# Performance work log

Measured on AMD Instinct MI355X. Metric: run time of the kernel, lower is better.

Reference implementation:

```python
import jax, jax.numpy as jnp
import numpy as np

N = 100000
E = 1600000
D_IN = 128
F = 128


def _glorot(key, shape, scale=1.0):
    fan_in, fan_out = shape
    std = jnp.sqrt(2.0 / (fan_in + fan_out))
    return jax.random.normal(key, shape, dtype=jnp.float32) * std * scale


def setup_inputs() -> dict:
    key = jax.random.key(0)
    ks = jax.random.split(key, 10)
    h = jax.random.normal(ks[0], (N, D_IN), dtype=jnp.float32)
    # ensure every node appears as a row (src) so degree >= 1 (no inf in deg**-0.5)
    src_extra = jax.random.randint(ks[1], (E - N,), 0, N, dtype=jnp.int32)
    edge_src = jnp.concatenate([jnp.arange(N, dtype=jnp.int32), src_extra])
    edge_dst = jax.random.randint(ks[2], (E,), 0, N, dtype=jnp.int32)
    # faithful to original: fake indices sampled in [0, E) (jnp indexing clamps)
    src_fake = jax.random.randint(ks[3], (E,), 0, E, dtype=jnp.int32)
    dst_fake = jax.random.randint(ks[4], (E,), 0, E, dtype=jnp.int32)
    w_gcn0 = _glorot(ks[5], (D_IN, F))
    w_gcn1 = _glorot(ks[6], (F, F))
    # small scale on rate0 head to keep exp(sum over F dims) finite in fp32
    w_rate0 = _glorot(ks[7], (F, F), scale=0.05)
    w_rate1 = _glorot(ks[8], (F, 1))
    w_alpha = _glorot(ks[9], (F, 1))
    return {"h": h, "w_gcn0": w_gcn0, "w_gcn1": w_gcn1, "w_rate0": w_rate0,
            "w_rate1": w_rate1, "w_alpha": w_alpha, "edge_src": edge_src,
            "edge_dst": edge_dst, "src_fake": src_fake, "dst_fake": dst_fake}


def _gcn(h, W, norm, edge_src, edge_dst):
    h = h * norm                     # [N, d] degree pre-norm
    h = h @ W                        # dense projection
    h = jax.ops.segment_sum(h[edge_dst], edge_src, num_segments=N)  # a @ h
    return h * norm                  # degree post-norm


def reference(h, w_gcn0, w_gcn1, w_rate0, w_rate1, w_alpha,
              edge_src, edge_dst, src_fake, dst_fake):
    ones = jnp.ones((E,), dtype=h.dtype)
    deg = jax.ops.segment_sum(ones, edge_src, num_segments=N)  # row sums of a
    norm = (deg ** -0.5)[:, None]

    h = _gcn(h, w_gcn0, norm, edge_src, edge_dst)
    h = _gcn(h, w_gcn1, norm, edge_src, edge_dst)

    rate0 = h @ w_rate0   # [N, F]
    rate1 = h @ w_rate1   # [N, 1]
    alpha = h @ w_alpha   # [N, 1]

    src, dst = edge_src, edge_dst
    rate0_real = jnp.exp((rate0[src] + rate0[dst]).sum(-1))
    rate1_real = jnp.exp((rate1[src] + rate1[dst]).sum(-1))
    alpha_real = jax.nn.sigmoid((alpha[src] * alpha[dst]).sum(-1) / alpha.shape[-1] ** 0.5)

    # faithful to original (including rate0+rate1 mix and /shape (not sqrt) in alpha_fake)
    rate0_fake = jnp.exp((rate0[src_fake] + rate1[dst_fake]).sum(-1))
    rate1_fake = jnp.exp((rate1[src_fake] + rate1[dst_fake]).sum(-1))
    alpha_fake = jax.nn.sigmoid((alpha[src] * alpha[dst_fake]).sum(-1) / alpha.shape[-1])

    return jnp.stack([rate0_real, rate1_real, alpha_real,
                      rate0_fake, rate1_fake, alpha_fake])  # [6, E]
```

## Files before the change

### kernel.cpp

```cpp
#include <hip/hip_runtime.h>
#include <math.h>

#define NN 100000
#define EE 1600000
#define KB 256
#define RR 391
#define CAP 8192


__global__ __launch_bounds__(1024) void k_pmat(const float* __restrict__ w_gcn0,
                                               const float* __restrict__ w_gcn1,
                                               const float* __restrict__ w_rate0,
                                               const float* __restrict__ w_rate1,
                                               const float* __restrict__ w_alpha,
                                               float* __restrict__ Pt0, float* __restrict__ Pt1,
                                               float* __restrict__ Pt2, int* __restrict__ gcur) {
    __shared__ float V0[128], V1[128], V2[128];
    __shared__ float Q0[128], Q1[128], Q2[128];
    int t = threadIdx.x;
    if (t < KB) gcur[t] = 0;
    int r = t >> 3, seg = t & 7;
    {
        const float* p = w_rate0 + r * 128 + seg * 16;
        float s = 0.f;
        #pragma unroll
        for (int k = 0; k < 16; ++k) s += p[k];
        s += __shfl_down(s, 4, 8); s += __shfl_down(s, 2, 8); s += __shfl_down(s, 1, 8);
        if (seg == 0) V0[r] = s;
    }
    if (t < 128) { V1[t] = w_rate1[t]; V2[t] = w_alpha[t]; }
    __syncthreads();
    {
        const float* p = w_gcn1 + r * 128 + seg * 16;
        float q0 = 0.f, q1 = 0.f, q2 = 0.f;
        #pragma unroll
        for (int k = 0; k < 16; ++k) {
            float w = p[k]; int j = seg * 16 + k;
            q0 += w * V0[j]; q1 += w * V1[j]; q2 += w * V2[j];
        }
        q0 += __shfl_down(q0, 4, 8); q0 += __shfl_down(q0, 2, 8); q0 += __shfl_down(q0, 1, 8);
        q1 += __shfl_down(q1, 4, 8); q1 += __shfl_down(q1, 2, 8); q1 += __shfl_down(q1, 1, 8);
        q2 += __shfl_down(q2, 4, 8); q2 += __shfl_down(q2, 2, 8); q2 += __shfl_down(q2, 1, 8);
        if (seg == 0) { Q0[r] = q0; Q1[r] = q1; Q2[r] = q2; }
    }
    __syncthreads();
    {
        const float* p = w_gcn0 + r * 128 + seg * 16;
        float q0 = 0.f, q1 = 0.f, q2 = 0.f;
        #pragma unroll
        for (int k = 0; k < 16; ++k) {
            float w = p[k]; int j = seg * 16 + k;
            q0 += w * Q0[j]; q1 += w * Q1[j]; q2 += w * Q2[j];
        }
        q0 += __shfl_down(q0, 4, 8); q0 += __shfl_down(q0, 2, 8); q0 += __shfl_down(q0, 1, 8);
        q1 += __shfl_down(q1, 4, 8); q1 += __shfl_down(q1, 2, 8); q1 += __shfl_down(q1, 1, 8);
        q2 += __shfl_down(q2, 4, 8); q2 += __shfl_down(q2, 2, 8); q2 += __shfl_down(q2, 1, 8);
        if (seg == 0) { Pt0[r] = q0; Pt1[r] = q1; Pt2[r] = q2; }
    }
}


__global__ __launch_bounds__(256) void k_part(const int* __restrict__ src, const int* __restrict__ dst,
                                              int* __restrict__ gcur, unsigned int* __restrict__ pk, int E) {
    __shared__ int cnt[KB];
    __shared__ int base[KB];
    int t = threadIdx.x;
    int e0 = blockIdx.x * 2048;
    cnt[t] = 0;
    __syncthreads();
    unsigned int pkv[8];
    int bkt[8];
    #pragma unroll
    for (int i = 0; i < 8; ++i) {
        int e = e0 + i * 256 + t;
        if (e < E) {
            int s = src[e];
            int d = dst[e];
            int b = s / RR;
            bkt[i] = b;
            pkv[i] = (unsigned int)d | ((unsigned int)(s - b * RR) << 17);
            atomicAdd(&cnt[b], 1);
        } else bkt[i] = -1;
    }
    __syncthreads();
    base[t] = cnt[t] ? atomicAdd(&gcur[t], cnt[t]) : 0;
    __syncthreads();
    cnt[t] = 0;
    __syncthreads();
    #pragma unroll
    for (int i = 0; i < 8; ++i) {
        if (bkt[i] >= 0) {
            int rr = atomicAdd(&cnt[bkt[i]], 1);
            int rel = base[bkt[i]] + rr;
            if (rel < CAP) pk[bkt[i] * CAP + rel] = pkv[i];
        }
    }
}


__global__ __launch_bounds__(1024) void k_cnt_proj(const unsigned int* __restrict__ pk,
                                                   const int* __restrict__ gcur,
                                                   const float* __restrict__ h,
                                                   const float* __restrict__ Pt0, const float* __restrict__ Pt1,
                                                   const float* __restrict__ Pt2,
                                                   float* __restrict__ nrm, float4* __restrict__ w4) {
    __shared__ int c[RR];
    __shared__ float s_nrm[RR];
    __shared__ float sP0[128], sP1[128], sP2[128];
    int b = blockIdx.x;
    int t = threadIdx.x;
    int nlo = b * RR;
    int nn = NN - nlo; if (nn > RR) nn = RR;
    if (nn <= 0) return;
    if (t < 128) { sP0[t] = Pt0[t]; sP1[t] = Pt1[t]; sP2[t] = Pt2[t]; }
    if (t < RR) c[t] = 0;
    __syncthreads();
    int P0 = b * CAP;
    int m = gcur[b]; if (m > CAP) m = CAP;
    for (int i = t; i < m; i += 1024) atomicAdd(&c[pk[P0 + i] >> 17], 1);
    __syncthreads();
    if (t < nn) {
        float nv = rsqrtf((float)c[t]);
        s_nrm[t] = nv;
        nrm[nlo + t] = nv;
    }
    __syncthreads();
    int hw = t >> 5;
    int l32 = t & 31;
    int c4 = l32 * 4;
    float4 c0 = *(const float4*)(sP0 + c4);
    float4 c1 = *(const float4*)(sP1 + c4);
    float4 c2 = *(const float4*)(sP2 + c4);
    for (int i0 = 0; i0 < nn; i0 += 32) {
        int i = i0 + hw;
        if (i >= nn) break;
        int node = nlo + i;
        float4 hv = *(const float4*)(h + (size_t)node * 128 + c4);
        float p0v = hv.x * c0.x + hv.y * c0.y + hv.z * c0.z + hv.w * c0.w;
        float p1v = hv.x * c1.x + hv.y * c1.y + hv.z * c1.z + hv.w * c1.w;
        float p2v = hv.x * c2.x + hv.y * c2.y + hv.z * c2.z + hv.w * c2.w;
        #pragma unroll
        for (int off = 16; off > 0; off >>= 1) {
            p0v += __shfl_down(p0v, off, 32);
            p1v += __shfl_down(p1v, off, 32);
            p2v += __shfl_down(p2v, off, 32);
        }
        if (l32 == 0) {
            float nv = s_nrm[i];
            w4[node] = make_float4(nv * p0v, nv * p1v, nv * p2v, 0.f);
        }
    }
}


template<int MODE>
__global__ __launch_bounds__(1024) void k_agg(const unsigned int* __restrict__ pk,
                                              const int* __restrict__ gcur,
                                              const float4* __restrict__ T, const float* __restrict__ nrm,
                                              float4* __restrict__ outv) {
    __shared__ float s0[RR], s1[RR], s2[RR];
    int b = blockIdx.x;
    int t = threadIdx.x;
    int nlo = b * RR;
    int nn = NN - nlo; if (nn > RR) nn = RR;
    if (nn <= 0) return;
    if (t < RR) { s0[t] = 0.f; s1[t] = 0.f; s2[t] = 0.f; }
    __syncthreads();
    int P0 = b * CAP;
    int m = gcur[b]; if (m > CAP) m = CAP;
    for (int i = t; i < m; i += 1024) {
        unsigned int w = pk[P0 + i];
        float4 v = T[w & 0x1FFFFu];
        int srel = (int)(w >> 17);
        atomicAdd(&s0[srel], v.x);
        atomicAdd(&s1[srel], v.y);
        atomicAdd(&s2[srel], v.z);
    }
    __syncthreads();
    for (int i = t; i < nn; i += 1024) {
        int node = nlo + i;
        float nv = nrm[node];
        float sc = (MODE == 1) ? nv * nv : nv;
        outv[node] = make_float4(sc * s0[i], sc * s1[i], sc * s2[i], 0.f);
    }
}


__global__ __launch_bounds__(256) void k_edge(const int* __restrict__ esrc, const int* __restrict__ edst,
                                              const int* __restrict__ sfake, const int* __restrict__ dfake,
                                              const float4* __restrict__ p4, float* __restrict__ out, int E) {
    int t = threadIdx.x;
    int e00 = blockIdx.x * 512 + t;
    #pragma unroll
    for (int k = 0; k < 2; ++k) {
        int e = e00 + k * 256;
        if (e < E) {
            int s = esrc[e], d = edst[e];
            int sf = sfake[e]; sf = sf < 0 ? 0 : (sf >= NN ? NN - 1 : sf);
            int df = dfake[e]; df = df < 0 ? 0 : (df >= NN ? NN - 1 : df);
            float4 ps = p4[s], pd = p4[d], psf = p4[sf], pdf = p4[df];
            out[e]                  = expf(ps.x + pd.x);
            out[(size_t)EE + e]     = expf(ps.y + pd.y);
            out[(size_t)2 * EE + e] = 1.f / (1.f + expf(-(ps.z * pd.z)));
            out[(size_t)3 * EE + e] = expf(psf.x + 128.f * pdf.y);
            out[(size_t)4 * EE + e] = expf(psf.y + pdf.y);
            out[(size_t)5 * EE + e] = 1.f / (1.f + expf(-(ps.z * pdf.z)));
        }
    }
}


extern "C" void kernel_launch(void* const* d_in, const int* in_sizes, int n_in,
                              void* d_out, int out_size, void* d_ws, size_t ws_size,
                              hipStream_t stream) {
    const float* h       = (const float*)d_in[0];
    const float* w_gcn0  = (const float*)d_in[1];
    const float* w_gcn1  = (const float*)d_in[2];
    const float* w_rate0 = (const float*)d_in[3];
    const float* w_rate1 = (const float*)d_in[4];
    const float* w_alpha = (const float*)d_in[5];
    const int* edge_src  = (const int*)d_in[6];
    const int* edge_dst  = (const int*)d_in[7];
    const int* src_fake  = (const int*)d_in[8];
    const int* dst_fake  = (const int*)d_in[9];
    float* out = (float*)d_out;

    const int E = EE;

    char* p = (char*)d_ws;
    auto alloc = [&](size_t bytes) {
        char* r = p;
        p += (bytes + 255) & ~(size_t)255;
        return r;
    };
    unsigned int* pk = (unsigned int*)alloc((size_t)KB * CAP * 4);
    int* gcur   = (int*)alloc(KB * 4);
    float* nrm  = (float*)alloc((size_t)NN * 4);
    float4* w4  = (float4*)alloc((size_t)NN * 16);
    float4* z4  = (float4*)alloc((size_t)NN * 16);
    float4* p4  = (float4*)alloc((size_t)NN * 16);
    float* Pt0  = (float*)alloc(512);
    float* Pt1  = (float*)alloc(512);
    float* Pt2  = (float*)alloc(512);

    k_pmat<<<1, 1024, 0, stream>>>(w_gcn0, w_gcn1, w_rate0, w_rate1, w_alpha, Pt0, Pt1, Pt2, gcur);
    k_part<<<(E + 2047) / 2048, 256, 0, stream>>>(edge_src, edge_dst, gcur, pk, E);
    k_cnt_proj<<<KB, 1024, 0, stream>>>(pk, gcur, h, Pt0, Pt1, Pt2, nrm, w4);
    k_agg<1><<<KB, 1024, 0, stream>>>(pk, gcur, w4, nrm, z4);
    k_agg<2><<<KB, 1024, 0, stream>>>(pk, gcur, z4, nrm, p4);
    k_edge<<<(E + 511) / 512, 256, 0, stream>>>(edge_src, edge_dst, src_fake, dst_fake, p4, out, E);
}
```

Baseline: 235.8 us.

## Overlap edge partition with h projection; vectorize edge kernel I/O

The edge partitioning and the h-projection now run in one launch, with blocks alternating between the two roles so the 51 MB h read overlaps the edge bucketing. Since the norm is not known yet at that point, it is stored in the w lane of u4 by the count kernel and applied inside the first aggregation. The aggregation loop is unrolled by two to keep more gathers in flight. The edge kernel uses int4 index loads and float4 output stores. The merged kernel removes the serial h read from the count kernel, but adds a branch per block and an extra multiply per gathered edge.

```diff
diff --git a/kernel.cpp b/kernel.cpp
--- a/kernel.cpp
+++ b/kernel.cpp
@@ -60,95 +60,103 @@
 }
 
 
-__global__ __launch_bounds__(256) void k_part(const int* __restrict__ src, const int* __restrict__ dst,
-                                              int* __restrict__ gcur, unsigned int* __restrict__ pk, int E) {
-    __shared__ int cnt[KB];
-    __shared__ int base[KB];
-    int t = threadIdx.x;
-    int e0 = blockIdx.x * 2048;
-    cnt[t] = 0;
-    __syncthreads();
-    unsigned int pkv[8];
-    int bkt[8];
-    #pragma unroll
-    for (int i = 0; i < 8; ++i) {
-        int e = e0 + i * 256 + t;
-        if (e < E) {
-            int s = src[e];
-            int d = dst[e];
-            int b = s / RR;
-            bkt[i] = b;
-            pkv[i] = (unsigned int)d | ((unsigned int)(s - b * RR) << 17);
-            atomicAdd(&cnt[b], 1);
-        } else bkt[i] = -1;
-    }
-    __syncthreads();
-    base[t] = cnt[t] ? atomicAdd(&gcur[t], cnt[t]) : 0;
-    __syncthreads();
-    cnt[t] = 0;
-    __syncthreads();
-    #pragma unroll
-    for (int i = 0; i < 8; ++i) {
-        if (bkt[i] >= 0) {
-            int rr = atomicAdd(&cnt[bkt[i]], 1);
-            int rel = base[bkt[i]] + rr;
-            if (rel < CAP) pk[bkt[i] * CAP + rel] = pkv[i];
-        }
-    }
-}
-
-
-__global__ __launch_bounds__(1024) void k_cnt_proj(const unsigned int* __restrict__ pk,
-                                                   const int* __restrict__ gcur,
+__global__ __launch_bounds__(512) void k_part_proj(const int* __restrict__ src, const int* __restrict__ dst,
+                                                   int* __restrict__ gcur, unsigned int* __restrict__ pk,
                                                    const float* __restrict__ h,
                                                    const float* __restrict__ Pt0, const float* __restrict__ Pt1,
                                                    const float* __restrict__ Pt2,
-                                                   float* __restrict__ nrm, float4* __restrict__ w4) {
+                                                   float4* __restrict__ u4) {
+    __shared__ int cnt[KB];
+    __shared__ int base[KB];
+    __shared__ float sP0[128], sP1[128], sP2[128];
+    int t = threadIdx.x;
+    int role = blockIdx.x & 1;
+    int id = blockIdx.x >> 1;
+
+    if (role == 0) {
+        if (t < KB) cnt[t] = 0;
+        __syncthreads();
+        int e0 = id * 4096;
+        unsigned int pkv[8];
+        int bkt[8];
+        #pragma unroll
+        for (int i = 0; i < 8; ++i) {
+            int e = e0 + i * 512 + t;
+            if (e < EE) {
+                int s = src[e];
+                int d = dst[e];
+                int b = s / RR;
+                bkt[i] = b;
+                pkv[i] = (unsigned int)d | ((unsigned int)(s - b * RR) << 17);
+                atomicAdd(&cnt[b], 1);
+            } else bkt[i] = -1;
+        }
+        __syncthreads();
+        if (t < KB) base[t] = cnt[t] ? atomicAdd(&gcur[t], cnt[t]) : 0;
+        __syncthreads();
+        if (t < KB) cnt[t] = 0;
+        __syncthreads();
+        #pragma unroll
+        for (int i = 0; i < 8; ++i) {
+            if (bkt[i] >= 0) {
+                int rr = atomicAdd(&cnt[bkt[i]], 1);
+                int rel = base[bkt[i]] + rr;
+                if (rel < CAP) pk[bkt[i] * CAP + rel] = pkv[i];
+            }
+        }
+    } else {
+        if (t < 128) { sP0[t] = Pt0[t]; sP1[t] = Pt1[t]; sP2[t] = Pt2[t]; }
+        __syncthreads();
+        int hw = t >> 5;
+        int l32 = t & 31;
+        int c4 = l32 * 4;
+        float4 c0 = *(const float4*)(sP0 + c4);
+        float4 c1 = *(const float4*)(sP1 + c4);
+        float4 c2 = *(const float4*)(sP2 + c4);
+        int nlo = id * 256;
+        for (int i0 = 0; i0 < 256; i0 += 16) {
+            int node = nlo + i0 + hw;
+            if (node < NN) {
+                float4 hv = *(const float4*)(h + (size_t)node * 128 + c4);
+                float p0v = hv.x * c0.x + hv.y * c0.y + hv.z * c0.z + hv.w * c0.w;
+                float p1v = hv.x * c1.x + hv.y * c1.y + hv.z * c1.z + hv.w * c1.w;
+                float p2v = hv.x * c2.x + hv.y * c2.y + hv.z * c2.z + hv.w * c2.w;
+                #pragma unroll
+                for (int off = 16; off > 0; off >>= 1) {
+                    p0v += __shfl_down(p0v, off, 32);
+                    p1v += __shfl_down(p1v, off, 32);
+                    p2v += __shfl_down(p2v, off, 32);
+                }
+                if (l32 == 0) {
+                    float* up = (float*)&u4[node];
+                    *(float2*)up = make_float2(p0v, p1v);
+                    up[2] = p2v;
+                }
+            }
+        }
+    }
+}
+
+
+__global__ __launch_bounds__(1024) void k_cnt(const unsigned int* __restrict__ pk,
+                                              const int* __restrict__ gcur,
+                                              float* __restrict__ nrm, float4* __restrict__ u4) {
     __shared__ int c[RR];
-    __shared__ float s_nrm[RR];
-    __shared__ float sP0[128], sP1[128], sP2[128];
     int b = blockIdx.x;
     int t = threadIdx.x;
     int nlo = b * RR;
     int nn = NN - nlo; if (nn > RR) nn = RR;
     if (nn <= 0) return;
-    if (t < 128) { sP0[t] = Pt0[t]; sP1[t] = Pt1[t]; sP2[t] = Pt2[t]; }
     if (t < RR) c[t] = 0;
     __syncthreads();
-    int P0 = b * CAP;
+    const unsigned int* P = pk + b * CAP;
     int m = gcur[b]; if (m > CAP) m = CAP;
-    for (int i = t; i < m; i += 1024) atomicAdd(&c[pk[P0 + i] >> 17], 1);
+    for (int i = t; i < m; i += 1024) atomicAdd(&c[P[i] >> 17], 1);
     __syncthreads();
     if (t < nn) {
         float nv = rsqrtf((float)c[t]);
-        s_nrm[t] = nv;
         nrm[nlo + t] = nv;
-    }
-    __syncthreads();
-    int hw = t >> 5;
-    int l32 = t & 31;
-    int c4 = l32 * 4;
-    float4 c0 = *(const float4*)(sP0 + c4);
-    float4 c1 = *(const float4*)(sP1 + c4);
-    float4 c2 = *(const float4*)(sP2 + c4);
-    for (int i0 = 0; i0 < nn; i0 += 32) {
-        int i = i0 + hw;
-        if (i >= nn) break;
-        int node = nlo + i;
-        float4 hv = *(const float4*)(h + (size_t)node * 128 + c4);
-        float p0v = hv.x * c0.x + hv.y * c0.y + hv.z * c0.z + hv.w * c0.w;
-        float p1v = hv.x * c1.x + hv.y * c1.y + hv.z * c1.z + hv.w * c1.w;
-        float p2v = hv.x * c2.x + hv.y * c2.y + hv.z * c2.z + hv.w * c2.w;
-        #pragma unroll
-        for (int off = 16; off > 0; off >>= 1) {
-            p0v += __shfl_down(p0v, off, 32);
-            p1v += __shfl_down(p1v, off, 32);
-            p2v += __shfl_down(p2v, off, 32);
-        }
-        if (l32 == 0) {
-            float nv = s_nrm[i];
-            w4[node] = make_float4(nv * p0v, nv * p1v, nv * p2v, 0.f);
-        }
+        ((float*)&u4[nlo + t])[3] = nv;
     }
 }
 
@@ -166,47 +174,71 @@
     if (nn <= 0) return;
     if (t < RR) { s0[t] = 0.f; s1[t] = 0.f; s2[t] = 0.f; }
     __syncthreads();
-    int P0 = b * CAP;
+    const unsigned int* P = pk + b * CAP;
     int m = gcur[b]; if (m > CAP) m = CAP;
-    for (int i = t; i < m; i += 1024) {
-        unsigned int w = pk[P0 + i];
-        float4 v = T[w & 0x1FFFFu];
-        int srel = (int)(w >> 17);
-        atomicAdd(&s0[srel], v.x);
-        atomicAdd(&s1[srel], v.y);
-        atomicAdd(&s2[srel], v.z);
-    }
-    __syncthreads();
-    for (int i = t; i < nn; i += 1024) {
-        int node = nlo + i;
-        float nv = nrm[node];
+    int i = t;
+    for (; i + 1024 < m; i += 2048) {
+        unsigned int wa = P[i];
+        unsigned int wb = P[i + 1024];
+        float4 va = T[wa & 0x1FFFFu];
+        float4 vb = T[wb & 0x1FFFFu];
+        float ax = va.x, ay = va.y, az = va.z;
+        float bx = vb.x, by = vb.y, bz = vb.z;
+        if (MODE == 1) { ax *= va.w; ay *= va.w; az *= va.w; bx *= vb.w; by *= vb.w; bz *= vb.w; }
+        int ra = (int)(wa >> 17), rb = (int)(wb >> 17);
+        atomicAdd(&s0[ra], ax); atomicAdd(&s1[ra], ay); atomicAdd(&s2[ra], az);
+        atomicAdd(&s0[rb], bx); atomicAdd(&s1[rb], by); atomicAdd(&s2[rb], bz);
+    }
+    if (i < m) {
+        unsigned int wa = P[i];
+        float4 va = T[wa & 0x1FFFFu];
+        float ax = va.x, ay = va.y, az = va.z;
+        if (MODE == 1) { ax *= va.w; ay *= va.w; az *= va.w; }
+        int ra = (int)(wa >> 17);
+        atomicAdd(&s0[ra], ax); atomicAdd(&s1[ra], ay); atomicAdd(&s2[ra], az);
+    }
+    __syncthreads();
+    for (int j = t; j < nn; j += 1024) {
+        float nv = nrm[nlo + j];
         float sc = (MODE == 1) ? nv * nv : nv;
-        outv[node] = make_float4(sc * s0[i], sc * s1[i], sc * s2[i], 0.f);
+        outv[nlo + j] = make_float4(sc * s0[j], sc * s1[j], sc * s2[j], 0.f);
     }
 }
 
 
 __global__ __launch_bounds__(256) void k_edge(const int* __restrict__ esrc, const int* __restrict__ edst,
                                               const int* __restrict__ sfake, const int* __restrict__ dfake,
-                                              const float4* __restrict__ p4, float* __restrict__ out, int E) {
-    int t = threadIdx.x;
-    int e00 = blockIdx.x * 512 + t;
+                                              const float4* __restrict__ p4, float* __restrict__ out) {
+    int t = threadIdx.x;
+    int e0 = blockIdx.x * 1024 + t * 4;
+    if (e0 >= EE) return;
+    int4 s4  = *(const int4*)(esrc + e0);
+    int4 d4  = *(const int4*)(edst + e0);
+    int4 sf4 = *(const int4*)(sfake + e0);
+    int4 df4 = *(const int4*)(dfake + e0);
+    int ss[4] = { s4.x, s4.y, s4.z, s4.w };
+    int dd[4] = { d4.x, d4.y, d4.z, d4.w };
+    int sf[4] = { sf4.x, sf4.y, sf4.z, sf4.w };
+    int df[4] = { df4.x, df4.y, df4.z, df4.w };
+    float o0[4], o1[4], o2[4], o3[4], o4[4], o5[4];
     #pragma unroll
-    for (int k = 0; k < 2; ++k) {
-        int e = e00 + k * 256;
-        if (e < E) {
-            int s = esrc[e], d = edst[e];
-            int sf = sfake[e]; sf = sf < 0 ? 0 : (sf >= NN ? NN - 1 : sf);
-            int df = dfake[e]; df = df < 0 ? 0 : (df >= NN ? NN - 1 : df);
-            float4 ps = p4[s], pd = p4[d], psf = p4[sf], pdf = p4[df];
-            out[e]                  = expf(ps.x + pd.x);
-            out[(size_t)EE + e]     = expf(ps.y + pd.y);
-            out[(size_t)2 * EE + e] = 1.f / (1.f + expf(-(ps.z * pd.z)));
-            out[(size_t)3 * EE + e] = expf(psf.x + 128.f * pdf.y);
-            out[(size_t)4 * EE + e] = expf(psf.y + pdf.y);
-            out[(size_t)5 * EE + e] = 1.f / (1.f + expf(-(ps.z * pdf.z)));
-        }
-    }
+    for (int j = 0; j < 4; ++j) {
+        int sfj = sf[j]; sfj = sfj < 0 ? 0 : (sfj >= NN ? NN - 1 : sfj);
+        int dfj = df[j]; dfj = dfj < 0 ? 0 : (dfj >= NN ? NN - 1 : dfj);
+        float4 ps = p4[ss[j]], pd = p4[dd[j]], psf = p4[sfj], pdf = p4[dfj];
+        o0[j] = expf(ps.x + pd.x);
+        o1[j] = expf(ps.y + pd.y);
+        o2[j] = 1.f / (1.f + expf(-(ps.z * pd.z)));
+        o3[j] = expf(psf.x + 128.f * pdf.y);
+        o4[j] = expf(psf.y + pdf.y);
+        o5[j] = 1.f / (1.f + expf(-(ps.z * pdf.z)));
+    }
+    *(float4*)(out + e0)                  = make_float4(o0[0], o0[1], o0[2], o0[3]);
+    *(float4*)(out + (size_t)EE + e0)     = make_float4(o1[0], o1[1], o1[2], o1[3]);
+    *(float4*)(out + (size_t)2 * EE + e0) = make_float4(o2[0], o2[1], o2[2], o2[3]);
+    *(float4*)(out + (size_t)3 * EE + e0) = make_float4(o3[0], o3[1], o3[2], o3[3]);
+    *(float4*)(out + (size_t)4 * EE + e0) = make_float4(o4[0], o4[1], o4[2], o4[3]);
+    *(float4*)(out + (size_t)5 * EE + e0) = make_float4(o5[0], o5[1], o5[2], o5[3]);
 }
 
 
@@ -225,8 +257,6 @@
     const int* dst_fake  = (const int*)d_in[9];
     float* out = (float*)d_out;
 
-    const int E = EE;
-
     char* p = (char*)d_ws;
     auto alloc = [&](size_t bytes) {
         char* r = p;
@@ -236,7 +266,7 @@
     unsigned int* pk = (unsigned int*)alloc((size_t)KB * CAP * 4);
     int* gcur   = (int*)alloc(KB * 4);
     float* nrm  = (float*)alloc((size_t)NN * 4);
-    float4* w4  = (float4*)alloc((size_t)NN * 16);
+    float4* u4  = (float4*)alloc((size_t)NN * 16);
     float4* z4  = (float4*)alloc((size_t)NN * 16);
     float4* p4  = (float4*)alloc((size_t)NN * 16);
     float* Pt0  = (float*)alloc(512);
@@ -244,9 +274,9 @@
     float* Pt2  = (float*)alloc(512);
 
     k_pmat<<<1, 1024, 0, stream>>>(w_gcn0, w_gcn1, w_rate0, w_rate1, w_alpha, Pt0, Pt1, Pt2, gcur);
-    k_part<<<(E + 2047) / 2048, 256, 0, stream>>>(edge_src, edge_dst, gcur, pk, E);
-    k_cnt_proj<<<KB, 1024, 0, stream>>>(pk, gcur, h, Pt0, Pt1, Pt2, nrm, w4);
-    k_agg<1><<<KB, 1024, 0, stream>>>(pk, gcur, w4, nrm, z4);
+    k_part_proj<<<782, 512, 0, stream>>>(edge_src, edge_dst, gcur, pk, h, Pt0, Pt1, Pt2, u4);
+    k_cnt<<<KB, 1024, 0, stream>>>(pk, gcur, nrm, u4);
+    k_agg<1><<<KB, 1024, 0, stream>>>(pk, gcur, u4, nrm, z4);
     k_agg<2><<<KB, 1024, 0, stream>>>(pk, gcur, z4, nrm, p4);
-    k_edge<<<(E + 511) / 512, 256, 0, stream>>>(edge_src, edge_dst, src_fake, dst_fake, p4, out, E);
-}
+    k_edge<<<(EE + 1023) / 1024, 256, 0, stream>>>(edge_src, edge_dst, src_fake, dst_fake, p4, out);
+}
```

Result: faster. 222.9 us (-5.5%).
